# Kernel tuning notes

Hardware: AMD Instinct MI355X
Metric: run time of the kernel (lower is better)

## Reference

```python
import jax, jax.numpy as jnp
import numpy as np

N = 100000
E = 1600000
D = 128


def setup_inputs() -> dict:
    key = jax.random.key(0)
    ks = jax.random.split(key, 6)
    x = jax.random.normal(ks[0], (N, D), dtype=jnp.float32)
    edge_row = jax.random.randint(ks[1], (E,), 0, N)
    edge_col = jax.random.randint(ks[2], (E,), 0, N)
    edge_val = jax.random.uniform(ks[3], (E,), dtype=jnp.float32)
    # Kaiming-ish init for the MLP weights
    W1 = jax.random.normal(ks[4], (D, D), dtype=jnp.float32) * (1.0 / np.sqrt(D))
    W2 = jax.random.normal(ks[5], (D, D), dtype=jnp.float32) * (1.0 / np.sqrt(D))
    b1 = jnp.zeros((D,), dtype=jnp.float32)
    b2 = jnp.zeros((D,), dtype=jnp.float32)
    eps = jnp.zeros((1,), dtype=jnp.float32)  # GIN eps, init 0
    bias = jnp.zeros((D,), dtype=jnp.float32)
    return {"x": x, "edge_row": edge_row, "edge_col": edge_col, "edge_val": edge_val,
            "W1": W1, "b1": b1, "W2": W2, "b2": b2, "eps": eps, "bias": bias}


def reference(x, edge_row, edge_col, edge_val, W1, b1, W2, b2, eps, bias):
    # sparse adj @ x : out[i] = sum_{edges (i,j)} val * x[j]
    agg = jax.ops.segment_sum(edge_val[:, None] * x[edge_col], edge_row, num_segments=N)
    h = (1.0 + eps) * x + agg                     # eps-scaled residual, [N, D]
    h = jax.nn.relu(h @ W1 + b1)                  # MLP layer 1
    h = jax.nn.relu(h @ W2 + b2)                  # MLP layer 2
    out = jax.nn.relu(h + bias)                   # bias + final relu
    return out
```

## Files before the change

kernel.cpp:

```cpp
#include <hip/hip_runtime.h>
#include <stdint.h>


static constexpr int NN = 100000;
static constexpr int NE = 1600000;
static constexpr int DD = 128;
static constexpr int NB = 196;
static constexpr int EPB = 4096;
static constexpr int PB = (NE + EPB - 1) / EPB;

typedef float f32x4 __attribute__((ext_vector_type(4)));
typedef short s16x8 __attribute__((ext_vector_type(8)));

__device__ __forceinline__ uint16_t f2bf(float f) {
  uint32_t u = __float_as_uint(f);
  u += 0x7fffu + ((u >> 16) & 1u);
  return (uint16_t)(u >> 16);
}
__device__ __forceinline__ float2 bf2f(uint32_t w) {
  float2 r;
  r.x = __uint_as_float(w << 16);
  r.y = __uint_as_float(w & 0xffff0000u);
  return r;
}

template <int WIDTH>
__device__ __forceinline__ int* scan_inc(int* s0, int* s1, int tid) {
  int* pin = s0;
  int* pout = s1;
  for (int off = 1; off < WIDTH; off <<= 1) {
    if (tid < WIDTH) pout[tid] = pin[tid] + ((tid >= off) ? pin[tid - off] : 0);
    __syncthreads();
    int* tmp = pin; pin = pout; pout = tmp;
  }
  return pin;
}

__global__ __launch_bounds__(256) void k_cvt(const float* __restrict__ x,
                                             uint32_t* __restrict__ xb, int nw) {
  int i = blockIdx.x * 256 + threadIdx.x;
  if (i < nw) {
    float2 v = ((const float2*)x)[i];
    xb[i] = (uint32_t)f2bf(v.x) | ((uint32_t)f2bf(v.y) << 16);
  }
}

__global__ __launch_bounds__(256) void k_init(int* __restrict__ bucket_tot,
                                              int2* __restrict__ es_pad) {
  int t = threadIdx.x;
  if (t < NB) bucket_tot[t] = 0;
  if (t < 8) es_pad[t] = int2{0, 0};
}

__global__ __launch_bounds__(1024) void k_part(const int* __restrict__ erow,
                                               const int* __restrict__ ecol,
                                               const float* __restrict__ eval,
                                               int2* __restrict__ part,
                                               int* __restrict__ runstart,
                                               int* __restrict__ bucket_tot) {
  __shared__ int hist[NB];
  __shared__ int cur[NB];
  __shared__ int s0[256], s1[256];
  __shared__ int2 stage[EPB];
  int t = threadIdx.x;
  int base = blockIdx.x * EPB;
  int cnt = min(EPB, NE - base);

  if (t < NB) hist[t] = 0;
  __syncthreads();

  int pb[4], pk[4], pv[4];
  #pragma unroll
  for (int j = 0; j < 4; ++j) {
    int i = t + j * 1024;
    pb[j] = -1;
    if (i < cnt) {
      int e = base + i;
      int r = erow[e];
      int b = r >> 9;
      pb[j] = b;
      pk[j] = ecol[e] | ((r & 511) << 17);
      pv[j] = __float_as_int(eval[e]);
      atomicAdd(&hist[b], 1);
    }
  }
  __syncthreads();

  if (t < 256) s0[t] = (t < NB) ? hist[t] : 0;
  __syncthreads();
  int* inc = scan_inc<256>(s0, s1, t);

  if (t < NB) {
    int h = hist[t];
    int st = inc[t] - h;
    cur[t] = st;
    runstart[blockIdx.x * (NB + 1) + t] = st;
    atomicAdd(&bucket_tot[t], h);
  }
  if (t == 0) runstart[blockIdx.x * (NB + 1) + NB] = cnt;
  __syncthreads();

  #pragma unroll
  for (int j = 0; j < 4; ++j) {
    if (pb[j] >= 0) {
      int off = atomicAdd(&cur[pb[j]], 1);
      stage[off] = int2{pk[j], pv[j]};
    }
  }
  __syncthreads();

  for (int i = t; i < cnt; i += 1024) part[base + i] = stage[i];
}

__global__ __launch_bounds__(256) void k_bbase(const int* __restrict__ tot,
                                               int* __restrict__ bbase) {
  __shared__ int s0[256], s1[256];
  int t = threadIdx.x;
  int v = (t < NB) ? tot[t] : 0;
  s0[t] = v;
  __syncthreads();
  int* inc = scan_inc<256>(s0, s1, t);
  if (t < NB) bbase[t] = inc[t] - v;
  if (t == NB - 1) bbase[NB] = inc[t];
}

__global__ __launch_bounds__(1024) void k_bucket(const int2* __restrict__ part,
                                                 const int* __restrict__ runstart,
                                                 const int* __restrict__ bbase,
                                                 int2* __restrict__ es,
                                                 int* __restrict__ rowptr) {
  __shared__ int cum[PB + 1];
  __shared__ int rbas[PB];
  __shared__ int hist[512];
  __shared__ int rps[512];
  __shared__ int cur[512];
  __shared__ int s0[512], s1[512];
  int b = blockIdx.x, t = threadIdx.x;

  int len = 0;
  if (t < PB) {
    int rs = runstart[t * (NB + 1) + b];
    int re = runstart[t * (NB + 1) + b + 1];
    len = re - rs;
    rbas[t] = t * EPB + rs;
  }
  if (t < 512) s0[t] = (t < PB) ? len : 0;
  __syncthreads();
  int* inc1 = scan_inc<512>(s0, s1, t);
  if (t < PB) cum[t] = inc1[t] - len;
  if (t == 0) cum[PB] = inc1[PB - 1];
  if (t < 512) hist[t] = 0;
  __syncthreads();

  int total = cum[PB];
  int base_out = bbase[b];

  int pk[16], pv[16];
  #pragma unroll
  for (int j = 0; j < 16; ++j) {
    int s = t + j * 1024;
    pk[j] = -1;
    if (s < total) {
      int lo = 0, hi = PB;
      while (hi - lo > 1) {
        int mid = (lo + hi) >> 1;
        if (cum[mid] <= s) lo = mid; else hi = mid;
      }
      int2 ev = part[rbas[lo] + (s - cum[lo])];
      pk[j] = ev.x; pv[j] = ev.y;
      atomicAdd(&hist[ev.x >> 17], 1);
    }
  }
  __syncthreads();

  if (t < 512) s0[t] = hist[t];
  __syncthreads();
  int* inc2 = scan_inc<512>(s0, s1, t);
  if (t < 512) {
    int ex = inc2[t] - hist[t];
    rps[t] = ex;
    cur[t] = ex;
  }
  __syncthreads();

  if (t < 512) {
    int row = b * 512 + t;
    if (row <= NN) rowptr[row] = base_out + rps[t];
  }

  #pragma unroll
  for (int j = 0; j < 16; ++j) {
    if (pk[j] >= 0) {
      int rib = pk[j] >> 17;
      int off = atomicAdd(&cur[rib], 1);
      es[base_out + off] = int2{pk[j] & 0x1FFFF, pv[j]};
    }
  }
}

__global__ __launch_bounds__(256) void k_agg(const uint32_t* __restrict__ xb,
                                             const int2* __restrict__ es,
                                             const int* __restrict__ rowptr,
                                             const float* __restrict__ eps,
                                             uint32_t* __restrict__ hb) {
  int wave = (blockIdx.x * 256 + threadIdx.x) >> 6;
  int lane = threadIdx.x & 63;
  if (wave >= NN) return;
  float e = 1.0f + eps[0];
  float2 h = bf2f(xb[(size_t)wave * 64 + lane]);
  h.x *= e; h.y *= e;
  int beg = rowptr[wave], end = rowptr[wave + 1];
  for (int k = beg; k < end; k += 8) {
    int2 ev[8];
    #pragma unroll
    for (int j = 0; j < 8; ++j) ev[j] = es[k + j];
    uint32_t xw[8];
    #pragma unroll
    for (int j = 0; j < 8; ++j) xw[j] = xb[(size_t)ev[j].x * 64 + lane];
    #pragma unroll
    for (int j = 0; j < 8; ++j) {
      float v = (k + j < end) ? __int_as_float(ev[j].y) : 0.0f;
      float2 xv = bf2f(xw[j]);
      h.x = fmaf(v, xv.x, h.x);
      h.y = fmaf(v, xv.y, h.y);
    }
  }
  hb[(size_t)wave * 64 + lane] = (uint32_t)f2bf(h.x) | ((uint32_t)f2bf(h.y) << 16);
}

template <bool FINAL>
__global__ __launch_bounds__(256, 2) void k_gemm(const uint16_t* __restrict__ A,
                                                 const float* __restrict__ W,
                                                 const float* __restrict__ bvec,
                                                 const float* __restrict__ bias2,
                                                 void* __restrict__ outp, int nrows) {
  __shared__ uint16_t wt[128 * 136];
  int tid = threadIdx.x;
  #pragma unroll 4
  for (int it = 0; it < 64; ++it) {
    int idx = tid + it * 256;
    int k = idx >> 7, n = idx & 127;
    wt[n * 136 + k] = f2bf(W[idx]);
  }
  __syncthreads();

  int wv = tid >> 6, l = tid & 63;
  int m16 = l & 15, qg = l >> 4;
  int w0 = blockIdx.x * 256 + wv * 64;

  int arow[4];
  #pragma unroll
  for (int mt = 0; mt < 4; ++mt) {
    int r = w0 + mt * 16 + m16;
    arow[mt] = (r < nrows) ? r : (nrows - 1);
  }

  f32x4 acc[4][8];
  #pragma unroll
  for (int mt = 0; mt < 4; ++mt)
    #pragma unroll
    for (int n0 = 0; n0 < 8; ++n0) acc[mt][n0] = f32x4{0.f, 0.f, 0.f, 0.f};

  #pragma unroll
  for (int k0 = 0; k0 < 128; k0 += 32) {
    s16x8 a[4];
    #pragma unroll
    for (int mt = 0; mt < 4; ++mt)
      a[mt] = *(const s16x8*)(A + (size_t)arow[mt] * 128 + k0 + qg * 8);
    #pragma unroll
    for (int n0 = 0; n0 < 8; ++n0) {
      s16x8 bfr = *(const s16x8*)(&wt[(n0 * 16 + m16) * 136 + k0 + qg * 8]);
      #pragma unroll
      for (int mt = 0; mt < 4; ++mt)
        acc[mt][n0] = __builtin_amdgcn_mfma_f32_16x16x32_bf16(a[mt], bfr, acc[mt][n0], 0, 0, 0);
    }
  }

  #pragma unroll
  for (int mt = 0; mt < 4; ++mt) {
    #pragma unroll
    for (int n0 = 0; n0 < 8; ++n0) {
      int col = n0 * 16 + m16;
      float bb = bvec[col];
      float b2 = FINAL ? bias2[col] : 0.0f;
      #pragma unroll
      for (int j = 0; j < 4; ++j) {
        int row = w0 + mt * 16 + qg * 4 + j;
        if (row < nrows) {
          float v = acc[mt][n0][j] + bb;
          v = fmaxf(v, 0.0f);
          if (FINAL) {
            v = fmaxf(v + b2, 0.0f);
            ((float*)outp)[(size_t)row * 128 + col] = v;
          } else {
            ((uint16_t*)outp)[(size_t)row * 128 + col] = f2bf(v);
          }
        }
      }
    }
  }
}

extern "C" void kernel_launch(void* const* d_in, const int* in_sizes, int n_in,
                              void* d_out, int out_size, void* d_ws, size_t ws_size,
                              hipStream_t stream) {
  const float* x    = (const float*)d_in[0];
  const int*   erow = (const int*)d_in[1];
  const int*   ecol = (const int*)d_in[2];
  const float* eval = (const float*)d_in[3];
  const float* W1   = (const float*)d_in[4];
  const float* b1   = (const float*)d_in[5];
  const float* W2   = (const float*)d_in[6];
  const float* b2   = (const float*)d_in[7];
  const float* eps  = (const float*)d_in[8];
  const float* bias = (const float*)d_in[9];

  char* w = (char*)d_ws;
  size_t off = 0;
  auto take = [&](size_t bytes) -> void* {
    void* p = w + off;
    off = (off + bytes + 255) & ~(size_t)255;
    return p;
  };
  uint32_t* xb     = (uint32_t*)take((size_t)NN * 64 * 4);
  uint32_t* hb     = (uint32_t*)take((size_t)NN * 64 * 4);
  uint16_t* h2b    = (uint16_t*)take((size_t)NN * DD * 2);
  int2*     part   = (int2*)h2b;
  int2*     es     = (int2*)take((size_t)(NE + 8) * 8);
  int*      rowptr = (int*)take((size_t)(NN + 1) * 4);
  int*      runst  = (int*)take((size_t)PB * (NB + 1) * 4);
  int*      btot   = (int*)take((size_t)(NB + 1) * 4);
  int*      bbase  = (int*)take((size_t)(NB + 1) * 4);
  (void)ws_size;

  k_cvt<<<(NN * 64 + 255) / 256, 256, 0, stream>>>(x, xb, NN * 64);
  k_init<<<1, 256, 0, stream>>>(btot, es + NE);
  k_part<<<PB, 1024, 0, stream>>>(erow, ecol, eval, part, runst, btot);
  k_bbase<<<1, 256, 0, stream>>>(btot, bbase);
  k_bucket<<<NB, 1024, 0, stream>>>(part, runst, bbase, es, rowptr);
  k_agg<<<(NN + 3) / 4, 256, 0, stream>>>(xb, es, rowptr, eps, hb);
  k_gemm<false><<<(NN + 255) / 256, 256, 0, stream>>>((const uint16_t*)hb, W1, b1,
                                                      nullptr, h2b, NN);
  k_gemm<true><<<(NN + 255) / 256, 256, 0, stream>>>(h2b, W2, b2, bias, d_out, NN);
}
```

Baseline: 270.5 us.

## Fuse the two MLP GEMMs, fold init and scan kernels, scalarize edge loads

The two GEMM launches become one kernel that keeps the first-layer activations in shared memory and reloads W2 into LDS, so the bf16 intermediate never makes a round trip through global memory. The init kernel is folded into a float4-vectorised conversion kernel, and the bucket-base scan now runs redundantly inside each bucket block, which removes two tiny launches. The aggregation kernel reads edge indices and row bounds through readfirstlane so they sit in scalar registers. In exchange each MLP block covers only 64 rows and must convert both weight matrices from fp32, which adds per-block setup work and lowers MFMA reuse per A load.

Result: faster. 262.7 us (-2.9%).

```diff
diff --git a/kernel.cpp b/kernel.cpp
--- a/kernel.cpp
+++ b/kernel.cpp
@@ -4,7 +4,6 @@
 
 static constexpr int NN = 100000;
 static constexpr int NE = 1600000;
-static constexpr int DD = 128;
 static constexpr int NB = 196;
 static constexpr int EPB = 4096;
 static constexpr int PB = (NE + EPB - 1) / EPB;
@@ -37,19 +36,22 @@
 }
 
 __global__ __launch_bounds__(256) void k_cvt(const float* __restrict__ x,
-                                             uint32_t* __restrict__ xb, int nw) {
+                                             uint32_t* __restrict__ xb, int nq,
+                                             int* __restrict__ btot,
+                                             int2* __restrict__ es_pad) {
   int i = blockIdx.x * 256 + threadIdx.x;
-  if (i < nw) {
-    float2 v = ((const float2*)x)[i];
-    xb[i] = (uint32_t)f2bf(v.x) | ((uint32_t)f2bf(v.y) << 16);
-  }
-}
-
-__global__ __launch_bounds__(256) void k_init(int* __restrict__ bucket_tot,
-                                              int2* __restrict__ es_pad) {
-  int t = threadIdx.x;
-  if (t < NB) bucket_tot[t] = 0;
-  if (t < 8) es_pad[t] = int2{0, 0};
+  if (i < nq) {
+    float4 v = ((const float4*)x)[i];
+    uint2 o;
+    o.x = (uint32_t)f2bf(v.x) | ((uint32_t)f2bf(v.y) << 16);
+    o.y = (uint32_t)f2bf(v.z) | ((uint32_t)f2bf(v.w) << 16);
+    ((uint2*)xb)[i] = o;
+  }
+  if (blockIdx.x == 0) {
+    int t = threadIdx.x;
+    if (t < NB) btot[t] = 0;
+    if (t < 8) es_pad[t] = int2{0, 0};
+  }
 }
 
 __global__ __launch_bounds__(1024) void k_part(const int* __restrict__ erow,
@@ -112,21 +114,9 @@
   for (int i = t; i < cnt; i += 1024) part[base + i] = stage[i];
 }
 
-__global__ __launch_bounds__(256) void k_bbase(const int* __restrict__ tot,
-                                               int* __restrict__ bbase) {
-  __shared__ int s0[256], s1[256];
-  int t = threadIdx.x;
-  int v = (t < NB) ? tot[t] : 0;
-  s0[t] = v;
-  __syncthreads();
-  int* inc = scan_inc<256>(s0, s1, t);
-  if (t < NB) bbase[t] = inc[t] - v;
-  if (t == NB - 1) bbase[NB] = inc[t];
-}
-
 __global__ __launch_bounds__(1024) void k_bucket(const int2* __restrict__ part,
                                                  const int* __restrict__ runstart,
-                                                 const int* __restrict__ bbase,
+                                                 const int* __restrict__ btot,
                                                  int2* __restrict__ es,
                                                  int* __restrict__ rowptr) {
   __shared__ int cum[PB + 1];
@@ -135,7 +125,18 @@
   __shared__ int rps[512];
   __shared__ int cur[512];
   __shared__ int s0[512], s1[512];
+  __shared__ int sbase;
   int b = blockIdx.x, t = threadIdx.x;
+
+  int bt = (t < NB) ? btot[t] : 0;
+  if (t < 512) s0[t] = (t < 256) ? ((t < NB) ? bt : 0) : 0;
+  __syncthreads();
+  {
+    int* incb = scan_inc<256>(s0, s1, t);
+    if (t == b) sbase = incb[b] - bt;
+  }
+  __syncthreads();
+  int base_out = sbase;
 
   int len = 0;
   if (t < PB) {
@@ -144,6 +145,7 @@
     len = re - rs;
     rbas[t] = t * EPB + rs;
   }
+  __syncthreads();
   if (t < 512) s0[t] = (t < PB) ? len : 0;
   __syncthreads();
   int* inc1 = scan_inc<512>(s0, s1, t);
@@ -153,7 +155,6 @@
   __syncthreads();
 
   int total = cum[PB];
-  int base_out = bbase[b];
 
   int pk[16], pv[16];
   #pragma unroll
@@ -203,99 +204,117 @@
                                              const int* __restrict__ rowptr,
                                              const float* __restrict__ eps,
                                              uint32_t* __restrict__ hb) {
-  int wave = (blockIdx.x * 256 + threadIdx.x) >> 6;
+  int wid = (blockIdx.x * 256 + threadIdx.x) >> 6;
+  int wave = __builtin_amdgcn_readfirstlane(wid);
   int lane = threadIdx.x & 63;
-  if (wave >= NN) return;
   float e = 1.0f + eps[0];
   float2 h = bf2f(xb[(size_t)wave * 64 + lane]);
   h.x *= e; h.y *= e;
-  int beg = rowptr[wave], end = rowptr[wave + 1];
+  int beg = __builtin_amdgcn_readfirstlane(rowptr[wave]);
+  int end = __builtin_amdgcn_readfirstlane(rowptr[wave + 1]);
   for (int k = beg; k < end; k += 8) {
-    int2 ev[8];
-    #pragma unroll
-    for (int j = 0; j < 8; ++j) ev[j] = es[k + j];
+    int scol[8]; float sval[8];
+    #pragma unroll
+    for (int j = 0; j < 8; ++j) {
+      int2 ev = es[k + j];
+      scol[j] = __builtin_amdgcn_readfirstlane(ev.x);
+      int vb = __builtin_amdgcn_readfirstlane(ev.y);
+      sval[j] = (k + j < end) ? __int_as_float(vb) : 0.0f;
+    }
     uint32_t xw[8];
     #pragma unroll
-    for (int j = 0; j < 8; ++j) xw[j] = xb[(size_t)ev[j].x * 64 + lane];
+    for (int j = 0; j < 8; ++j)
+      xw[j] = xb[((size_t)scol[j] << 6) + lane];
     #pragma unroll
     for (int j = 0; j < 8; ++j) {
-      float v = (k + j < end) ? __int_as_float(ev[j].y) : 0.0f;
       float2 xv = bf2f(xw[j]);
-      h.x = fmaf(v, xv.x, h.x);
-      h.y = fmaf(v, xv.y, h.y);
+      h.x = fmaf(sval[j], xv.x, h.x);
+      h.y = fmaf(sval[j], xv.y, h.y);
     }
   }
   hb[(size_t)wave * 64 + lane] = (uint32_t)f2bf(h.x) | ((uint32_t)f2bf(h.y) << 16);
 }
 
-template <bool FINAL>
-__global__ __launch_bounds__(256, 2) void k_gemm(const uint16_t* __restrict__ A,
-                                                 const float* __restrict__ W,
-                                                 const float* __restrict__ bvec,
-                                                 const float* __restrict__ bias2,
-                                                 void* __restrict__ outp, int nrows) {
+__global__ __launch_bounds__(256, 3) void k_mlp(const uint16_t* __restrict__ A,
+                                                const float* __restrict__ W1,
+                                                const float* __restrict__ b1,
+                                                const float* __restrict__ W2,
+                                                const float* __restrict__ b2,
+                                                const float* __restrict__ bias,
+                                                float* __restrict__ out, int nrows) {
   __shared__ uint16_t wt[128 * 136];
+  __shared__ uint16_t h1[64 * 136];
   int tid = threadIdx.x;
+
   #pragma unroll 4
   for (int it = 0; it < 64; ++it) {
     int idx = tid + it * 256;
-    int k = idx >> 7, n = idx & 127;
-    wt[n * 136 + k] = f2bf(W[idx]);
+    wt[(idx & 127) * 136 + (idx >> 7)] = f2bf(W1[idx]);
   }
   __syncthreads();
 
   int wv = tid >> 6, l = tid & 63;
   int m16 = l & 15, qg = l >> 4;
-  int w0 = blockIdx.x * 256 + wv * 64;
-
-  int arow[4];
-  #pragma unroll
-  for (int mt = 0; mt < 4; ++mt) {
-    int r = w0 + mt * 16 + m16;
-    arow[mt] = (r < nrows) ? r : (nrows - 1);
-  }
-
-  f32x4 acc[4][8];
-  #pragma unroll
-  for (int mt = 0; mt < 4; ++mt)
-    #pragma unroll
-    for (int n0 = 0; n0 < 8; ++n0) acc[mt][n0] = f32x4{0.f, 0.f, 0.f, 0.f};
+  int r0 = blockIdx.x * 64 + wv * 16;
+  int arow = r0 + m16;
+  if (arow >= nrows) arow = nrows - 1;
+
+  f32x4 acc[8];
+  #pragma unroll
+  for (int n0 = 0; n0 < 8; ++n0) acc[n0] = f32x4{0.f, 0.f, 0.f, 0.f};
 
   #pragma unroll
   for (int k0 = 0; k0 < 128; k0 += 32) {
-    s16x8 a[4];
-    #pragma unroll
-    for (int mt = 0; mt < 4; ++mt)
-      a[mt] = *(const s16x8*)(A + (size_t)arow[mt] * 128 + k0 + qg * 8);
+    s16x8 a = *(const s16x8*)(A + (size_t)arow * 128 + k0 + qg * 8);
     #pragma unroll
     for (int n0 = 0; n0 < 8; ++n0) {
       s16x8 bfr = *(const s16x8*)(&wt[(n0 * 16 + m16) * 136 + k0 + qg * 8]);
-      #pragma unroll
-      for (int mt = 0; mt < 4; ++mt)
-        acc[mt][n0] = __builtin_amdgcn_mfma_f32_16x16x32_bf16(a[mt], bfr, acc[mt][n0], 0, 0, 0);
-    }
-  }
-
-  #pragma unroll
-  for (int mt = 0; mt < 4; ++mt) {
+      acc[n0] = __builtin_amdgcn_mfma_f32_16x16x32_bf16(a, bfr, acc[n0], 0, 0, 0);
+    }
+  }
+
+  #pragma unroll
+  for (int n0 = 0; n0 < 8; ++n0) {
+    int col = n0 * 16 + m16;
+    float bb = b1[col];
+    #pragma unroll
+    for (int j = 0; j < 4; ++j) {
+      int lr = wv * 16 + qg * 4 + j;
+      h1[lr * 136 + col] = f2bf(fmaxf(acc[n0][j] + bb, 0.0f));
+    }
+  }
+  __syncthreads();
+
+  #pragma unroll 4
+  for (int it = 0; it < 64; ++it) {
+    int idx = tid + it * 256;
+    wt[(idx & 127) * 136 + (idx >> 7)] = f2bf(W2[idx]);
+  }
+  #pragma unroll
+  for (int n0 = 0; n0 < 8; ++n0) acc[n0] = f32x4{0.f, 0.f, 0.f, 0.f};
+  __syncthreads();
+
+  #pragma unroll
+  for (int k0 = 0; k0 < 128; k0 += 32) {
+    s16x8 a = *(const s16x8*)(&h1[(wv * 16 + m16) * 136 + k0 + qg * 8]);
     #pragma unroll
     for (int n0 = 0; n0 < 8; ++n0) {
-      int col = n0 * 16 + m16;
-      float bb = bvec[col];
-      float b2 = FINAL ? bias2[col] : 0.0f;
-      #pragma unroll
-      for (int j = 0; j < 4; ++j) {
-        int row = w0 + mt * 16 + qg * 4 + j;
-        if (row < nrows) {
-          float v = acc[mt][n0][j] + bb;
-          v = fmaxf(v, 0.0f);
-          if (FINAL) {
-            v = fmaxf(v + b2, 0.0f);
-            ((float*)outp)[(size_t)row * 128 + col] = v;
-          } else {
-            ((uint16_t*)outp)[(size_t)row * 128 + col] = f2bf(v);
-          }
-        }
+      s16x8 bfr = *(const s16x8*)(&wt[(n0 * 16 + m16) * 136 + k0 + qg * 8]);
+      acc[n0] = __builtin_amdgcn_mfma_f32_16x16x32_bf16(a, bfr, acc[n0], 0, 0, 0);
+    }
+  }
+
+  #pragma unroll
+  for (int n0 = 0; n0 < 8; ++n0) {
+    int col = n0 * 16 + m16;
+    float bb = b2[col];
+    float b3 = bias[col];
+    #pragma unroll
+    for (int j = 0; j < 4; ++j) {
+      int row = r0 + qg * 4 + j;
+      if (row < nrows) {
+        float v = fmaxf(fmaxf(acc[n0][j] + bb, 0.0f) + b3, 0.0f);
+        out[(size_t)row * 128 + col] = v;
       }
     }
   }
@@ -324,22 +343,17 @@
   };
   uint32_t* xb     = (uint32_t*)take((size_t)NN * 64 * 4);
   uint32_t* hb     = (uint32_t*)take((size_t)NN * 64 * 4);
-  uint16_t* h2b    = (uint16_t*)take((size_t)NN * DD * 2);
-  int2*     part   = (int2*)h2b;
+  int2*     part   = (int2*)take((size_t)NE * 8);
   int2*     es     = (int2*)take((size_t)(NE + 8) * 8);
   int*      rowptr = (int*)take((size_t)(NN + 1) * 4);
   int*      runst  = (int*)take((size_t)PB * (NB + 1) * 4);
   int*      btot   = (int*)take((size_t)(NB + 1) * 4);
-  int*      bbase  = (int*)take((size_t)(NB + 1) * 4);
   (void)ws_size;
 
-  k_cvt<<<(NN * 64 + 255) / 256, 256, 0, stream>>>(x, xb, NN * 64);
-  k_init<<<1, 256, 0, stream>>>(btot, es + NE);
+  k_cvt<<<(NN * 32 + 255) / 256, 256, 0, stream>>>(x, xb, NN * 32, btot, es + NE);
   k_part<<<PB, 1024, 0, stream>>>(erow, ecol, eval, part, runst, btot);
-  k_bbase<<<1, 256, 0, stream>>>(btot, bbase);
-  k_bucket<<<NB, 1024, 0, stream>>>(part, runst, bbase, es, rowptr);
+  k_bucket<<<NB, 1024, 0, stream>>>(part, runst, btot, es, rowptr);
   k_agg<<<(NN + 3) / 4, 256, 0, stream>>>(xb, es, rowptr, eps, hb);
-  k_gemm<false><<<(NN + 255) / 256, 256, 0, stream>>>((const uint16_t*)hb, W1, b1,
-                                                      nullptr, h2b, NN);
-  k_gemm<true><<<(NN + 255) / 256, 256, 0, stream>>>(h2b, W2, b2, bias, d_out, NN);
-}
+  k_mlp<<<(NN + 63) / 64, 256, 0, stream>>>((const uint16_t*)hb, W1, b1, W2, b2,
+                                            bias, (float*)d_out, NN);
+}
```
